# Kernel optimization log

Hardware: AMD Instinct MI355X
Metric: run time of the kernel (lower is better)

The kernel has to match this reference:

```python
import jax, jax.numpy as jnp
import numpy as np

BLOCKSIZE = 64  # elements per quantization block


def setup_inputs() -> dict:
    key = jax.random.key(0)
    k1, k2, k3, k4 = jax.random.split(key, 4)
    out_features, in_features = 11008, 4096
    tokens = 8192  # batch 4 * seq 2048
    n = out_features * in_features
    x = jax.random.normal(k1, (tokens, in_features), dtype=jnp.float32)
    codes = jax.random.randint(k2, (n,), 0, 16, dtype=jnp.int32)
    absmax = jax.random.uniform(k3, (n // BLOCKSIZE,), dtype=jnp.float32)
    # NF4-style codebook (16 quantization levels)
    codebook = jnp.array(
        [-1.0, -0.6962, -0.5251, -0.3949, -0.2844, -0.1848, -0.0911, 0.0,
         0.0796, 0.1609, 0.2461, 0.3379, 0.4407, 0.5626, 0.7230, 1.0],
        dtype=jnp.float32)
    bias = jax.random.normal(k4, (out_features,), dtype=jnp.float32)
    return {"x": x, "codes": codes, "absmax": absmax,
            "codebook": codebook, "bias": bias}


def reference(x, codes, absmax, codebook, bias):
    out_features, in_features = 11008, 4096
    # Dequantize: codebook lookup, then per-block scale.  [n] -> [out, in]
    w = codebook[codes].reshape(-1, BLOCKSIZE) * absmax[:, None]
    w = w.reshape(out_features, in_features)
    # y = x @ W.T + b
    y = jnp.einsum('ti,oi->to', x, w) + bias
    return y
```

## Files before the change

### kernel.cpp

```cpp
#include <hip/hip_runtime.h>
#include <hip/hip_bf16.h>
#include <stdint.h>

#define TOKENS 8192
#define OUTF   11008
#define INF    4096
#define NCODES (45088768)

typedef __bf16 bf16x8 __attribute__((ext_vector_type(8)));
typedef float  f32x4  __attribute__((ext_vector_type(4)));

__device__ __forceinline__ unsigned short f32_to_bf16_rne(float f) {
    union { float f; unsigned int u; } v; v.f = f;
    unsigned int u = v.u;
    unsigned int r = u + 0x7fffu + ((u >> 16) & 1u);
    return (unsigned short)(r >> 16);
}

__global__ __launch_bounds__(256) void dequant_w(const int* __restrict__ codes,
                                                 const float* __restrict__ absmax,
                                                 const float* __restrict__ codebook,
                                                 unsigned short* __restrict__ wq) {
    __shared__ float cb[16];
    if (threadIdx.x < 16) cb[threadIdx.x] = codebook[threadIdx.x];
    __syncthreads();
    size_t idx = ((size_t)blockIdx.x * 256 + threadIdx.x) * 8;
    float am = absmax[idx >> 6];
    const int4* cp = (const int4*)(codes + idx);
    int4 c0 = cp[0];
    int4 c1 = cp[1];
    union { unsigned short s[8]; uint4 v; } u;
    u.s[0] = f32_to_bf16_rne(cb[c0.x] * am);
    u.s[1] = f32_to_bf16_rne(cb[c0.y] * am);
    u.s[2] = f32_to_bf16_rne(cb[c0.z] * am);
    u.s[3] = f32_to_bf16_rne(cb[c0.w] * am);
    u.s[4] = f32_to_bf16_rne(cb[c1.x] * am);
    u.s[5] = f32_to_bf16_rne(cb[c1.y] * am);
    u.s[6] = f32_to_bf16_rne(cb[c1.z] * am);
    u.s[7] = f32_to_bf16_rne(cb[c1.w] * am);
    *(uint4*)(wq + idx) = u.v;
}

__global__ __launch_bounds__(256) void cast_x(const float* __restrict__ x,
                                              unsigned short* __restrict__ xq) {
    size_t idx = ((size_t)blockIdx.x * 256 + threadIdx.x) * 8;
    float4 a = *(const float4*)(x + idx);
    float4 b = *(const float4*)(x + idx + 4);
    union { unsigned short s[8]; uint4 v; } u;
    u.s[0] = f32_to_bf16_rne(a.x);
    u.s[1] = f32_to_bf16_rne(a.y);
    u.s[2] = f32_to_bf16_rne(a.z);
    u.s[3] = f32_to_bf16_rne(a.w);
    u.s[4] = f32_to_bf16_rne(b.x);
    u.s[5] = f32_to_bf16_rne(b.y);
    u.s[6] = f32_to_bf16_rne(b.z);
    u.s[7] = f32_to_bf16_rne(b.w);
    *(uint4*)(xq + idx) = u.v;
}

#define BM 128
#define BN 128
#define BK 32

__global__ __launch_bounds__(256) void gemm_bf16(const unsigned short* __restrict__ Xb,
                                                 const unsigned short* __restrict__ Wb,
                                                 const float* __restrict__ bias,
                                                 float* __restrict__ out) {
    __shared__ __align__(16) unsigned short lA[BM * BK];
    __shared__ __align__(16) unsigned short lB[BN * BK];

    const int bid  = blockIdx.x;
    const int xcd  = bid & 7;
    const int slot = bid >> 3;
    const int mpart = xcd >> 1;
    const int npart = xcd & 1;
    const int sub  = slot >> 7;
    const int rem  = slot & 127;
    const int mloc = rem & 15;
    const int nloc = sub * 8 + (rem >> 4);
    const int m0 = (mpart * 16 + mloc) * BM;
    const int n0 = (npart * 43 + nloc) * BN;

    const int tid  = threadIdx.x;
    const int lane = tid & 63;
    const int wave = tid >> 6;
    const int wm = (wave >> 1) * 64;
    const int wn = (wave & 1) * 64;

    f32x4 acc[4][4];
#pragma unroll
    for (int i = 0; i < 4; i++)
#pragma unroll
        for (int j = 0; j < 4; j++)
#pragma unroll
            for (int r = 0; r < 4; r++) acc[i][j][r] = 0.0f;

    const int ch0 = tid, ch1 = tid + 256;
    const int rA0 = ch0 >> 2, kA0 = (ch0 & 3) * 8;
    const int rA1 = ch1 >> 2, kA1 = (ch1 & 3) * 8;
    const unsigned short* gA0 = Xb + (size_t)(m0 + rA0) * INF + kA0;
    const unsigned short* gA1 = Xb + (size_t)(m0 + rA1) * INF + kA1;
    const unsigned short* gB0 = Wb + (size_t)(n0 + rA0) * INF + kA0;
    const unsigned short* gB1 = Wb + (size_t)(n0 + rA1) * INF + kA1;
    unsigned short* lA0 = &lA[ch0 * 8];
    unsigned short* lA1 = &lA[ch1 * 8];
    unsigned short* lB0 = &lB[ch0 * 8];
    unsigned short* lB1 = &lB[ch1 * 8];

    const int frow = lane & 15;
    const int kgrp = (lane >> 4) * 8;

    for (int k0 = 0; k0 < INF; k0 += BK) {
        __syncthreads();
        __builtin_amdgcn_global_load_lds((const __attribute__((address_space(1))) void*)(gA0 + k0),
                                         (__attribute__((address_space(3))) void*)lA0, 16, 0, 0);
        __builtin_amdgcn_global_load_lds((const __attribute__((address_space(1))) void*)(gA1 + k0),
                                         (__attribute__((address_space(3))) void*)lA1, 16, 0, 0);
        __builtin_amdgcn_global_load_lds((const __attribute__((address_space(1))) void*)(gB0 + k0),
                                         (__attribute__((address_space(3))) void*)lB0, 16, 0, 0);
        __builtin_amdgcn_global_load_lds((const __attribute__((address_space(1))) void*)(gB1 + k0),
                                         (__attribute__((address_space(3))) void*)lB1, 16, 0, 0);
        __syncthreads();

        bf16x8 af[4], bfr[4];
#pragma unroll
        for (int i = 0; i < 4; i++)
            af[i] = *(const bf16x8*)&lA[(wm + i * 16 + frow) * BK + kgrp];
#pragma unroll
        for (int j = 0; j < 4; j++)
            bfr[j] = *(const bf16x8*)&lB[(wn + j * 16 + frow) * BK + kgrp];
#pragma unroll
        for (int i = 0; i < 4; i++)
#pragma unroll
            for (int j = 0; j < 4; j++)
                acc[i][j] = __builtin_amdgcn_mfma_f32_16x16x32_bf16(af[i], bfr[j], acc[i][j], 0, 0, 0);
    }

    const int crow = (lane >> 4) * 4;
    const int ccol = lane & 15;
#pragma unroll
    for (int j = 0; j < 4; j++) {
        const int n = n0 + wn + j * 16 + ccol;
        const float bv = bias[n];
#pragma unroll
        for (int i = 0; i < 4; i++) {
            const int m = m0 + wm + i * 16 + crow;
#pragma unroll
            for (int r = 0; r < 4; r++)
                out[(size_t)(m + r) * OUTF + n] = acc[i][j][r] + bv;
        }
    }
}

__global__ __launch_bounds__(256) void fused_fallback(const float* __restrict__ x,
                                                      const int* __restrict__ codes,
                                                      const float* __restrict__ absmax,
                                                      const float* __restrict__ codebook,
                                                      const float* __restrict__ bias,
                                                      float* __restrict__ out) {
    __shared__ float xs[64][17];
    __shared__ float wsm[64][17];
    __shared__ float cb[16];
    const int tid = threadIdx.x;
    if (tid < 16) cb[tid] = codebook[tid];
    const int m0 = blockIdx.y * 64, n0 = blockIdx.x * 64;
    float acc[4][4] = {};
    const int tr = tid >> 4, tc = tid & 15;
    for (int k0 = 0; k0 < INF; k0 += 16) {
        __syncthreads();
#pragma unroll
        for (int i = 0; i < 4; i++) {
            int e = i * 256 + tid;
            int r = e >> 4, c = e & 15;
            xs[r][c] = x[(size_t)(m0 + r) * INF + k0 + c];
            size_t widx = (size_t)(n0 + r) * INF + k0 + c;
            wsm[r][c] = cb[codes[widx]] * absmax[widx >> 6];
        }
        __syncthreads();
#pragma unroll
        for (int kk = 0; kk < 16; kk++) {
            float xv[4], wv[4];
#pragma unroll
            for (int i = 0; i < 4; i++) xv[i] = xs[tr * 4 + i][kk];
#pragma unroll
            for (int j = 0; j < 4; j++) wv[j] = wsm[tc * 4 + j][kk];
#pragma unroll
            for (int i = 0; i < 4; i++)
#pragma unroll
                for (int j = 0; j < 4; j++) acc[i][j] += xv[i] * wv[j];
        }
    }
#pragma unroll
    for (int i = 0; i < 4; i++)
#pragma unroll
        for (int j = 0; j < 4; j++) {
            int m = m0 + tr * 4 + i, n = n0 + tc * 4 + j;
            out[(size_t)m * OUTF + n] = acc[i][j] + bias[n];
        }
}

extern "C" void kernel_launch(void* const* d_in, const int* in_sizes, int n_in,
                              void* d_out, int out_size, void* d_ws, size_t ws_size,
                              hipStream_t stream) {
    const float* x        = (const float*)d_in[0];
    const int*   codes    = (const int*)d_in[1];
    const float* absmax   = (const float*)d_in[2];
    const float* codebook = (const float*)d_in[3];
    const float* bias     = (const float*)d_in[4];
    float* out = (float*)d_out;

    const size_t wbytes = (size_t)NCODES * 2;
    const size_t xbytes = (size_t)TOKENS * INF * 2;

    if (ws_size >= wbytes + xbytes) {
        unsigned short* wq = (unsigned short*)d_ws;
        unsigned short* xq = (unsigned short*)((char*)d_ws + wbytes);
        dequant_w<<<NCODES / 2048, 256, 0, stream>>>(codes, absmax, codebook, wq);
        cast_x<<<(TOKENS * INF) / 2048, 256, 0, stream>>>(x, xq);
        gemm_bf16<<<dim3((OUTF / BN) * (TOKENS / BM)), 256, 0, stream>>>(xq, wq, bias, out);
    } else {
        dim3 grid(OUTF / 64, TOKENS / 64);
        fused_fallback<<<grid, 256, 0, stream>>>(x, codes, absmax, codebook, bias, out);
    }
}
```

Measured before the change: 1.432 ms.

## Rewrite bf16 GEMM with 256x256 tiles and 8-phase double-buffered LDS pipeline

Replaces the 128x128x32 single-buffered GEMM with a 256x256x64 tile kernel using 8 waves, double-buffered LDS filled by direct global-to-LDS loads, and XOR-swizzled LDS layout. The main loop interleaves staged loads for the next k-tiles with MFMA quadrants under explicit barriers, waitcnts and priority raises, so memory latency overlaps compute. It also remaps blocks to XCDs by M tiles. The 128KB LDS footprint limits occupancy to one block per CU, and the hand-scheduled waitcnt counts make correctness fragile.

```diff
diff --git a/kernel.cpp b/kernel.cpp
--- a/kernel.cpp
+++ b/kernel.cpp
@@ -58,98 +58,155 @@
     *(uint4*)(xq + idx) = u.v;
 }
 
-#define BM 128
-#define BN 128
-#define BK 32
-
-__global__ __launch_bounds__(256) void gemm_bf16(const unsigned short* __restrict__ Xb,
-                                                 const unsigned short* __restrict__ Wb,
-                                                 const float* __restrict__ bias,
-                                                 float* __restrict__ out) {
-    __shared__ __align__(16) unsigned short lA[BM * BK];
-    __shared__ __align__(16) unsigned short lB[BN * BK];
+#define BM 256
+#define BN 256
+#define BK 64
+
+#define GLLDS(SRC, DST)                                                                   \
+    __builtin_amdgcn_global_load_lds((const __attribute__((address_space(1))) void*)(SRC),\
+                                     (__attribute__((address_space(3))) void*)(DST), 16, 0, 0)
+
+#define STAGE_A(KT, HALF, BUF) do {                                                       \
+    const unsigned short* _s = gA + (size_t)(HALF) * (128 * INF) + (size_t)(KT) * BK;     \
+    GLLDS(_s,                   &lA[BUF][(HALF) * 8192 + tid * 8]);                       \
+    GLLDS(_s + (size_t)64 * INF, &lA[BUF][(HALF) * 8192 + tid * 8 + 4096]); } while (0)
+
+#define STAGE_B(KT, HALF, BUF) do {                                                       \
+    const unsigned short* _s = gB + (size_t)(HALF) * (128 * INF) + (size_t)(KT) * BK;     \
+    GLLDS(_s,                   &lB[BUF][(HALF) * 8192 + tid * 8]);                       \
+    GLLDS(_s + (size_t)64 * INF, &lB[BUF][(HALF) * 8192 + tid * 8 + 4096]); } while (0)
+
+#define LOAD_A(BUF, MH) do { _Pragma("unroll")                                            \
+    for (int i = 0; i < 4; ++i) {                                                         \
+        a[i][0] = *(const bf16x8*)&lA[BUF][(MH) * 8192 + i * 1024 + aRow + sw0];          \
+        a[i][1] = *(const bf16x8*)&lA[BUF][(MH) * 8192 + i * 1024 + aRow + sw1]; } } while (0)
+
+#define LOAD_B(BUF, NH) do { _Pragma("unroll")                                            \
+    for (int j = 0; j < 2; ++j) {                                                         \
+        b[j][0] = *(const bf16x8*)&lB[BUF][(NH) * 8192 + j * 1024 + bRow + sw0];          \
+        b[j][1] = *(const bf16x8*)&lB[BUF][(NH) * 8192 + j * 1024 + bRow + sw1]; } } while (0)
+
+#define MFMA_Q(MH, NH) do {                                                               \
+    __builtin_amdgcn_s_setprio(1);                                                        \
+    _Pragma("unroll") for (int kc = 0; kc < 2; ++kc)                                      \
+    _Pragma("unroll") for (int i = 0; i < 4; ++i)                                         \
+    _Pragma("unroll") for (int j = 0; j < 2; ++j)                                         \
+        acc[MH][i][NH][j] = __builtin_amdgcn_mfma_f32_16x16x32_bf16(                      \
+            a[i][kc], b[j][kc], acc[MH][i][NH][j], 0, 0, 0);                              \
+    __builtin_amdgcn_s_setprio(0); } while (0)
+
+#define BARR   __builtin_amdgcn_s_barrier()
+#define LGKM0  asm volatile("s_waitcnt lgkmcnt(0)" ::: "memory")
+#define VMC(N) asm volatile("s_waitcnt vmcnt(" #N ")" ::: "memory")
+
+__global__ __launch_bounds__(512, 2) void gemm_bf16_8p(const unsigned short* __restrict__ Xb,
+                                                       const unsigned short* __restrict__ Wb,
+                                                       const float* __restrict__ bias,
+                                                       float* __restrict__ out) {
+    __shared__ __align__(16) unsigned short lA[2][BM * BK];
+    __shared__ __align__(16) unsigned short lB[2][BN * BK];
 
     const int bid  = blockIdx.x;
     const int xcd  = bid & 7;
-    const int slot = bid >> 3;
-    const int mpart = xcd >> 1;
-    const int npart = xcd & 1;
-    const int sub  = slot >> 7;
-    const int rem  = slot & 127;
-    const int mloc = rem & 15;
-    const int nloc = sub * 8 + (rem >> 4);
-    const int m0 = (mpart * 16 + mloc) * BM;
-    const int n0 = (npart * 43 + nloc) * BN;
+    const int loc  = bid >> 3;
+    const int mt   = xcd * 4 + (loc & 3);
+    const int nt   = loc >> 2;
+    const int m0   = mt * BM;
+    const int n0   = nt * BN;
 
     const int tid  = threadIdx.x;
     const int lane = tid & 63;
     const int wave = tid >> 6;
-    const int wm = (wave >> 1) * 64;
-    const int wn = (wave & 1) * 64;
-
-    f32x4 acc[4][4];
-#pragma unroll
-    for (int i = 0; i < 4; i++)
-#pragma unroll
-        for (int j = 0; j < 4; j++)
-#pragma unroll
-            for (int r = 0; r < 4; r++) acc[i][j][r] = 0.0f;
-
-    const int ch0 = tid, ch1 = tid + 256;
-    const int rA0 = ch0 >> 2, kA0 = (ch0 & 3) * 8;
-    const int rA1 = ch1 >> 2, kA1 = (ch1 & 3) * 8;
-    const unsigned short* gA0 = Xb + (size_t)(m0 + rA0) * INF + kA0;
-    const unsigned short* gA1 = Xb + (size_t)(m0 + rA1) * INF + kA1;
-    const unsigned short* gB0 = Wb + (size_t)(n0 + rA0) * INF + kA0;
-    const unsigned short* gB1 = Wb + (size_t)(n0 + rA1) * INF + kA1;
-    unsigned short* lA0 = &lA[ch0 * 8];
-    unsigned short* lA1 = &lA[ch1 * 8];
-    unsigned short* lB0 = &lB[ch0 * 8];
-    unsigned short* lB1 = &lB[ch1 * 8];
+    const int wm_l = wave >> 2;
+    const int wn_l = wave & 3;
 
     const int frow = lane & 15;
-    const int kgrp = (lane >> 4) * 8;
-
-    for (int k0 = 0; k0 < INF; k0 += BK) {
-        __syncthreads();
-        __builtin_amdgcn_global_load_lds((const __attribute__((address_space(1))) void*)(gA0 + k0),
-                                         (__attribute__((address_space(3))) void*)lA0, 16, 0, 0);
-        __builtin_amdgcn_global_load_lds((const __attribute__((address_space(1))) void*)(gA1 + k0),
-                                         (__attribute__((address_space(3))) void*)lA1, 16, 0, 0);
-        __builtin_amdgcn_global_load_lds((const __attribute__((address_space(1))) void*)(gB0 + k0),
-                                         (__attribute__((address_space(3))) void*)lB0, 16, 0, 0);
-        __builtin_amdgcn_global_load_lds((const __attribute__((address_space(1))) void*)(gB1 + k0),
-                                         (__attribute__((address_space(3))) void*)lB1, 16, 0, 0);
-        __syncthreads();
-
-        bf16x8 af[4], bfr[4];
-#pragma unroll
-        for (int i = 0; i < 4; i++)
-            af[i] = *(const bf16x8*)&lA[(wm + i * 16 + frow) * BK + kgrp];
-#pragma unroll
-        for (int j = 0; j < 4; j++)
-            bfr[j] = *(const bf16x8*)&lB[(wn + j * 16 + frow) * BK + kgrp];
-#pragma unroll
-        for (int i = 0; i < 4; i++)
-#pragma unroll
-            for (int j = 0; j < 4; j++)
-                acc[i][j] = __builtin_amdgcn_mfma_f32_16x16x32_bf16(af[i], bfr[j], acc[i][j], 0, 0, 0);
+    const int klan = lane >> 4;
+    const int f7   = lane & 7;
+    const int sw0  = ((klan)     ^ f7) * 8;
+    const int sw1  = ((klan + 4) ^ f7) * 8;
+    const int aRow = (wm_l * 64 + frow) * BK;
+    const int bRow = (wn_l * 32 + frow) * BK;
+
+    const int rl   = tid >> 3;
+    const int gsw  = (tid & 7) ^ (rl & 7);
+    const unsigned short* gA = Xb + (size_t)(m0 + rl) * INF + gsw * 8;
+    const unsigned short* gB = Wb + (size_t)(n0 + rl) * INF + gsw * 8;
+
+    f32x4 acc[2][4][2][2];
+#pragma unroll
+    for (int mh = 0; mh < 2; ++mh)
+#pragma unroll
+        for (int i = 0; i < 4; ++i)
+#pragma unroll
+            for (int nh = 0; nh < 2; ++nh)
+#pragma unroll
+                for (int j = 0; j < 2; ++j)
+#pragma unroll
+                    for (int r = 0; r < 4; ++r) acc[mh][i][nh][j][r] = 0.0f;
+
+    bf16x8 a[4][2], b[2][2];
+
+    STAGE_A(0, 0, 0); STAGE_B(0, 1, 0); STAGE_A(0, 1, 0); STAGE_B(0, 0, 0);
+    STAGE_A(1, 0, 1); STAGE_B(1, 1, 1); STAGE_A(1, 1, 1);
+    VMC(6);
+    BARR;
+
+    for (int it = 0; it < 31; ++it) {
+        const int kt1 = 2 * it + 1, kt2 = 2 * it + 2, kt3 = 2 * it + 3;
+        LOAD_A(0, 0); LOAD_B(0, 0); STAGE_B(kt1, 0, 1);
+        BARR; LGKM0; MFMA_Q(0, 0); BARR;
+        LOAD_B(0, 1); STAGE_A(kt2, 0, 0);
+        BARR; LGKM0; MFMA_Q(0, 1); BARR;
+        LOAD_A(0, 1); STAGE_B(kt2, 1, 0);
+        BARR; LGKM0; MFMA_Q(1, 1); BARR;
+        LOAD_B(0, 0); STAGE_A(kt2, 1, 0);
+        BARR; LGKM0; MFMA_Q(1, 0); VMC(6); BARR;
+        LOAD_A(1, 0); LOAD_B(1, 0); STAGE_B(kt2, 0, 0);
+        BARR; LGKM0; MFMA_Q(0, 0); BARR;
+        LOAD_B(1, 1); STAGE_A(kt3, 0, 1);
+        BARR; LGKM0; MFMA_Q(0, 1); BARR;
+        LOAD_A(1, 1); STAGE_B(kt3, 1, 1);
+        BARR; LGKM0; MFMA_Q(1, 1); BARR;
+        LOAD_B(1, 0); STAGE_A(kt3, 1, 1);
+        BARR; LGKM0; MFMA_Q(1, 0); VMC(6); BARR;
     }
+
+    LOAD_A(0, 0); LOAD_B(0, 0); STAGE_B(63, 0, 1);
+    BARR; LGKM0; MFMA_Q(0, 0); BARR;
+    LOAD_B(0, 1);
+    BARR; LGKM0; MFMA_Q(0, 1); BARR;
+    LOAD_A(0, 1);
+    BARR; LGKM0; MFMA_Q(1, 1); BARR;
+    LOAD_B(0, 0);
+    BARR; LGKM0; MFMA_Q(1, 0); VMC(0); BARR;
+    LOAD_A(1, 0); LOAD_B(1, 0);
+    BARR; LGKM0; MFMA_Q(0, 0); BARR;
+    LOAD_B(1, 1);
+    BARR; LGKM0; MFMA_Q(0, 1); BARR;
+    LOAD_A(1, 1);
+    BARR; LGKM0; MFMA_Q(1, 1); BARR;
+    LOAD_B(1, 0);
+    BARR; LGKM0; MFMA_Q(1, 0);
 
     const int crow = (lane >> 4) * 4;
     const int ccol = lane & 15;
 #pragma unroll
-    for (int j = 0; j < 4; j++) {
-        const int n = n0 + wn + j * 16 + ccol;
-        const float bv = bias[n];
-#pragma unroll
-        for (int i = 0; i < 4; i++) {
-            const int m = m0 + wm + i * 16 + crow;
-#pragma unroll
-            for (int r = 0; r < 4; r++)
-                out[(size_t)(m + r) * OUTF + n] = acc[i][j][r] + bv;
-        }
-    }
+    for (int mh = 0; mh < 2; ++mh)
+#pragma unroll
+        for (int nh = 0; nh < 2; ++nh)
+#pragma unroll
+            for (int j = 0; j < 2; ++j) {
+                const int n = n0 + nh * 128 + wn_l * 32 + j * 16 + ccol;
+                const float bv = bias[n];
+#pragma unroll
+                for (int i = 0; i < 4; ++i) {
+                    const int m = m0 + mh * 128 + wm_l * 64 + i * 16 + crow;
+#pragma unroll
+                    for (int r = 0; r < 4; ++r)
+                        out[(size_t)(m + r) * OUTF + n] = acc[mh][i][nh][j][r] + bv;
+                }
+            }
 }
 
 __global__ __launch_bounds__(256) void fused_fallback(const float* __restrict__ x,
@@ -217,7 +274,7 @@
         unsigned short* xq = (unsigned short*)((char*)d_ws + wbytes);
         dequant_w<<<NCODES / 2048, 256, 0, stream>>>(codes, absmax, codebook, wq);
         cast_x<<<(TOKENS * INF) / 2048, 256, 0, stream>>>(x, xq);
-        gemm_bf16<<<dim3((OUTF / BN) * (TOKENS / BM)), 256, 0, stream>>>(xq, wq, bias, out);
+        gemm_bf16_8p<<<dim3((TOKENS / BM) * (OUTF / BN)), 512, 0, stream>>>(xq, wq, bias, out);
     } else {
         dim3 grid(OUTF / 64, TOKENS / 64);
         fused_fallback<<<grid, 256, 0, stream>>>(x, codes, absmax, codebook, bias, out);
```

Measured after the change: 1.252 ms. 1.14x faster.
